# Kernel tuning notes

Measured on AMD Instinct MI355X. Metric: run time of the kernel, lower is better.

Reference implementation:

```python
import jax, jax.numpy as jnp
import numpy as np
from jax import lax

M = 4194304      # total ray samples
N_RAYS = 16384   # number of rays
INTERVAL = 0.5
ALPHA_INIT = 1e-6


def setup_inputs() -> dict:
    key = jax.random.key(0)
    k1, k2, k3 = jax.random.split(key, 3)
    density = jax.random.normal(k1, (M,), dtype=jnp.float32)
    rgb_raw = jax.random.normal(k2, (M, 3), dtype=jnp.float32)
    # act_shift buffer: log(1/(1-alpha_init) - 1)
    shift = jnp.full((1,), np.log(1.0 / (1.0 - ALPHA_INIT) - 1.0), dtype=jnp.float32)
    ray_id = jnp.sort(jax.random.randint(k3, (M,), 0, N_RAYS, dtype=jnp.int32))
    return {"density": density, "rgb_raw": rgb_raw, "shift": shift,
            "ray_id": ray_id, "N": N_RAYS}


def _seg_comb(a, b):
    # associative operator for segmented product scan: (prod, reset_flag)
    pa, fa = a
    pb, fb = b
    return jnp.where(fb, pb, pa * pb), fa | fb


def reference(density, rgb_raw, shift, ray_id, N):
    # Raw2Alpha: alpha = 1 - exp(-softplus(density + shift) * interval)
    s = jax.nn.softplus(density + shift[0]) * INTERVAL   # [M], >= 0
    alpha = -jnp.expm1(-s)                                # 1 - exp(-s), stable
    om = jnp.exp(-s)                                      # 1 - alpha, exact

    # Alphas2Weights: per-ray transmittance scan over variable-length segments.
    first = jnp.concatenate([jnp.ones((1,), bool), ray_id[1:] != ray_id[:-1]])
    # inclusive segmented cumprod of (1 - alpha)
    Tin, _ = lax.associative_scan(_seg_comb, (om, first))
    # exclusive transmittance: T_i = prod of (1-alpha_j) for j earlier in same ray
    T = jnp.where(first, 1.0, jnp.concatenate([jnp.ones((1,), om.dtype), Tin[:-1]]))
    weights = alpha * T                                   # [M]
    # leftover transmittance per ray (1 for rays with no samples)
    alphainv_last = jax.ops.segment_prod(om, ray_id, num_segments=N)  # [N]

    # alpha compositing of colors against a white background
    rgb = jax.nn.sigmoid(rgb_raw)                          # [M,3]
    rgb_marched = (jax.ops.segment_sum(weights[:, None] * rgb, ray_id, num_segments=N)
                   + alphainv_last[:, None])               # [N,3]
    return rgb_marched
```

## Files before the change

kernel.cpp:

```cpp
#include <hip/hip_runtime.h>
#include <math.h>


#define INTERVAL 0.5f

__global__ __launch_bounds__(256) void voxel_march_kernel(
    const float* __restrict__ density,
    const float* __restrict__ rgb_raw,
    const float* __restrict__ shift,
    const int*   __restrict__ ray_id,
    float* __restrict__ out,
    int M, int N)
{
    const int lane = threadIdx.x & 63;
    const int wave = threadIdx.x >> 6;
    const int ray  = blockIdx.x * 4 + wave;
    if (ray >= N) return;

    const float sh = shift[0];

    int target = ray + (lane >= 32 ? 1 : 0);
    int lo = 0, len = M;
    while (len > 0) {
        int half = len >> 1;
        int mid  = lo + half;
        if (ray_id[mid] < target) { lo = mid + 1; len -= half + 1; }
        else                      { len = half; }
    }
    const int begin = __shfl(lo, 0, 64);
    const int end   = __shfl(lo, 32, 64);

    float carry = 1.0f;
    float acc0 = 0.0f, acc1 = 0.0f, acc2 = 0.0f;

    for (int base = (begin & ~3); base < end; base += 256) {
        const int b4 = base + 4 * lane;

        float d0, d1, d2, d3;
        float r[12];

        if (b4 >= begin && b4 + 3 < end) {
            const float4 dd = *(const float4*)(density + b4);
            d0 = dd.x; d1 = dd.y; d2 = dd.z; d3 = dd.w;
            const float4* rp = (const float4*)(rgb_raw + 3 * b4);
            float4 a0 = rp[0], a1 = rp[1], a2 = rp[2];
            r[0]=a0.x; r[1]=a0.y; r[2]=a0.z; r[3]=a0.w;
            r[4]=a1.x; r[5]=a1.y; r[6]=a1.z; r[7]=a1.w;
            r[8]=a2.x; r[9]=a2.y; r[10]=a2.z; r[11]=a2.w;
        } else {
            #pragma unroll
            for (int k = 0; k < 4; ++k) {
                const int j = b4 + k;
                const bool act = (j >= begin) && (j < end);
                float dk = act ? density[j] : -1e30f;
                if (k == 0) d0 = dk; else if (k == 1) d1 = dk;
                else if (k == 2) d2 = dk; else d3 = dk;
                r[3*k+0] = act ? rgb_raw[3*j+0] : 0.0f;
                r[3*k+1] = act ? rgb_raw[3*j+1] : 0.0f;
                r[3*k+2] = act ? rgb_raw[3*j+2] : 0.0f;
            }
        }

        const float om0 = __builtin_amdgcn_rsqf(1.0f + __expf(d0 + sh));
        const float om1 = __builtin_amdgcn_rsqf(1.0f + __expf(d1 + sh));
        const float om2 = __builtin_amdgcn_rsqf(1.0f + __expf(d2 + sh));
        const float om3 = __builtin_amdgcn_rsqf(1.0f + __expf(d3 + sh));
        const float al0 = 1.0f - om0, al1 = 1.0f - om1;
        const float al2 = 1.0f - om2, al3 = 1.0f - om3;

        const float lp = (om0 * om1) * (om2 * om3);
        float p = lp;
        #pragma unroll
        for (int off = 1; off < 64; off <<= 1) {
            float q = __shfl_up(p, off, 64);
            if (lane >= off) p *= q;
        }
        float excl = __shfl_up(p, 1, 64);
        if (lane == 0) excl = 1.0f;

        float t = carry * excl;
        const float w0 = al0 * t; t *= om0;
        const float w1 = al1 * t; t *= om1;
        const float w2 = al2 * t; t *= om2;
        const float w3 = al3 * t;

        acc0 += w0 * __builtin_amdgcn_rcpf(1.0f + __expf(-r[0]))
              + w1 * __builtin_amdgcn_rcpf(1.0f + __expf(-r[3]))
              + w2 * __builtin_amdgcn_rcpf(1.0f + __expf(-r[6]))
              + w3 * __builtin_amdgcn_rcpf(1.0f + __expf(-r[9]));
        acc1 += w0 * __builtin_amdgcn_rcpf(1.0f + __expf(-r[1]))
              + w1 * __builtin_amdgcn_rcpf(1.0f + __expf(-r[4]))
              + w2 * __builtin_amdgcn_rcpf(1.0f + __expf(-r[7]))
              + w3 * __builtin_amdgcn_rcpf(1.0f + __expf(-r[10]));
        acc2 += w0 * __builtin_amdgcn_rcpf(1.0f + __expf(-r[2]))
              + w1 * __builtin_amdgcn_rcpf(1.0f + __expf(-r[5]))
              + w2 * __builtin_amdgcn_rcpf(1.0f + __expf(-r[8]))
              + w3 * __builtin_amdgcn_rcpf(1.0f + __expf(-r[11]));

        carry *= __shfl(p, 63, 64);
    }

    #pragma unroll
    for (int off = 32; off > 0; off >>= 1) {
        acc0 += __shfl_down(acc0, off, 64);
        acc1 += __shfl_down(acc1, off, 64);
        acc2 += __shfl_down(acc2, off, 64);
    }

    if (lane == 0) {
        out[3 * ray + 0] = acc0 + carry;
        out[3 * ray + 1] = acc1 + carry;
        out[3 * ray + 2] = acc2 + carry;
    }
}

extern "C" void kernel_launch(void* const* d_in, const int* in_sizes, int n_in,
                              void* d_out, int out_size, void* d_ws, size_t ws_size,
                              hipStream_t stream)
{
    const float* density = (const float*)d_in[0];
    const float* rgb_raw = (const float*)d_in[1];
    const float* shift   = (const float*)d_in[2];
    const int*   ray_id  = (const int*)d_in[3];
    float* out = (float*)d_out;

    const int M = in_sizes[0];
    const int N = out_size / 3;

    const int rays_per_block = 4;
    const int blocks = (N + rays_per_block - 1) / rays_per_block;
    voxel_march_kernel<<<blocks, 256, 0, stream>>>(density, rgb_raw, shift, ray_id,
                                                   out, M, N);
}
```

Before: 129.8 us.

## Precompute ray segment starts in a separate kernel and use branchless vector loads

Adds a pre-pass kernel that writes each ray's start offset into workspace, replacing the per-wave binary search over ray_id. The main loop now always does clamped float4 loads and masks invalid samples with selects instead of a scalar fallback path. This removes the dependent global-memory latency chain of the search and the divergent edge handling. In exchange it adds a second launch, a full read of ray_id, and a workspace dependency with a fallback when the workspace is too small.

```diff
diff --git a/kernel.cpp b/kernel.cpp
--- a/kernel.cpp
+++ b/kernel.cpp
@@ -2,13 +2,30 @@
 #include <math.h>
 
 
-#define INTERVAL 0.5f
+__device__ __forceinline__ float sigm(float x) {
+    return __builtin_amdgcn_rcpf(1.0f + __expf(-x));
+}
 
+__global__ __launch_bounds__(256) void seg_starts_kernel(
+    const int* __restrict__ ray_id, int* __restrict__ starts, int M, int N)
+{
+    const int i = blockIdx.x * 256 + threadIdx.x;
+    if (i >= M) return;
+    const int cur  = ray_id[i];
+    const int prev = (i == 0) ? -1 : ray_id[i - 1];
+    for (int r = prev + 1; r <= cur; ++r) starts[r] = i;
+    if (i == M - 1) {
+        for (int r = cur + 1; r <= N; ++r) starts[r] = M;
+    }
+}
+
+template <bool USE_STARTS>
 __global__ __launch_bounds__(256) void voxel_march_kernel(
     const float* __restrict__ density,
     const float* __restrict__ rgb_raw,
     const float* __restrict__ shift,
     const int*   __restrict__ ray_id,
+    const int*   __restrict__ starts,
     float* __restrict__ out,
     int M, int N)
 {
@@ -19,47 +36,42 @@
 
     const float sh = shift[0];
 
-    int target = ray + (lane >= 32 ? 1 : 0);
-    int lo = 0, len = M;
-    while (len > 0) {
-        int half = len >> 1;
-        int mid  = lo + half;
-        if (ray_id[mid] < target) { lo = mid + 1; len -= half + 1; }
-        else                      { len = half; }
+    int begin, end;
+    if (USE_STARTS) {
+        begin = starts[ray];
+        end   = starts[ray + 1];
+    } else {
+        int target = ray + (lane >= 32 ? 1 : 0);
+        int lo = 0, len = M;
+        while (len > 0) {
+            int half = len >> 1;
+            int mid  = lo + half;
+            if (ray_id[mid] < target) { lo = mid + 1; len -= half + 1; }
+            else                      { len = half; }
+        }
+        begin = __shfl(lo, 0, 64);
+        end   = __shfl(lo, 32, 64);
     }
-    const int begin = __shfl(lo, 0, 64);
-    const int end   = __shfl(lo, 32, 64);
 
     float carry = 1.0f;
     float acc0 = 0.0f, acc1 = 0.0f, acc2 = 0.0f;
 
     for (int base = (begin & ~3); base < end; base += 256) {
         const int b4 = base + 4 * lane;
+        const int ba = min(b4, M - 4);
 
-        float d0, d1, d2, d3;
-        float r[12];
+        const float4 dd = *(const float4*)(density + ba);
+        const float4* rp = (const float4*)(rgb_raw + 3 * ba);
+        const float4 c0 = rp[0], c1 = rp[1], c2 = rp[2];
 
-        if (b4 >= begin && b4 + 3 < end) {
-            const float4 dd = *(const float4*)(density + b4);
-            d0 = dd.x; d1 = dd.y; d2 = dd.z; d3 = dd.w;
-            const float4* rp = (const float4*)(rgb_raw + 3 * b4);
-            float4 a0 = rp[0], a1 = rp[1], a2 = rp[2];
-            r[0]=a0.x; r[1]=a0.y; r[2]=a0.z; r[3]=a0.w;
-            r[4]=a1.x; r[5]=a1.y; r[6]=a1.z; r[7]=a1.w;
-            r[8]=a2.x; r[9]=a2.y; r[10]=a2.z; r[11]=a2.w;
-        } else {
-            #pragma unroll
-            for (int k = 0; k < 4; ++k) {
-                const int j = b4 + k;
-                const bool act = (j >= begin) && (j < end);
-                float dk = act ? density[j] : -1e30f;
-                if (k == 0) d0 = dk; else if (k == 1) d1 = dk;
-                else if (k == 2) d2 = dk; else d3 = dk;
-                r[3*k+0] = act ? rgb_raw[3*j+0] : 0.0f;
-                r[3*k+1] = act ? rgb_raw[3*j+1] : 0.0f;
-                r[3*k+2] = act ? rgb_raw[3*j+2] : 0.0f;
-            }
-        }
+        const bool v0 = (b4 + 0 >= begin) & (b4 + 0 < end);
+        const bool v1 = (b4 + 1 >= begin) & (b4 + 1 < end);
+        const bool v2 = (b4 + 2 >= begin) & (b4 + 2 < end);
+        const bool v3 = (b4 + 3 >= begin) & (b4 + 3 < end);
+        const float d0 = v0 ? dd.x : -1e30f;
+        const float d1 = v1 ? dd.y : -1e30f;
+        const float d2 = v2 ? dd.z : -1e30f;
+        const float d3 = v3 ? dd.w : -1e30f;
 
         const float om0 = __builtin_amdgcn_rsqf(1.0f + __expf(d0 + sh));
         const float om1 = __builtin_amdgcn_rsqf(1.0f + __expf(d1 + sh));
@@ -84,18 +96,9 @@
         const float w2 = al2 * t; t *= om2;
         const float w3 = al3 * t;
 
-        acc0 += w0 * __builtin_amdgcn_rcpf(1.0f + __expf(-r[0]))
-              + w1 * __builtin_amdgcn_rcpf(1.0f + __expf(-r[3]))
-              + w2 * __builtin_amdgcn_rcpf(1.0f + __expf(-r[6]))
-              + w3 * __builtin_amdgcn_rcpf(1.0f + __expf(-r[9]));
-        acc1 += w0 * __builtin_amdgcn_rcpf(1.0f + __expf(-r[1]))
-              + w1 * __builtin_amdgcn_rcpf(1.0f + __expf(-r[4]))
-              + w2 * __builtin_amdgcn_rcpf(1.0f + __expf(-r[7]))
-              + w3 * __builtin_amdgcn_rcpf(1.0f + __expf(-r[10]));
-        acc2 += w0 * __builtin_amdgcn_rcpf(1.0f + __expf(-r[2]))
-              + w1 * __builtin_amdgcn_rcpf(1.0f + __expf(-r[5]))
-              + w2 * __builtin_amdgcn_rcpf(1.0f + __expf(-r[8]))
-              + w3 * __builtin_amdgcn_rcpf(1.0f + __expf(-r[11]));
+        acc0 += w0 * sigm(c0.x) + w1 * sigm(c0.w) + w2 * sigm(c1.z) + w3 * sigm(c2.y);
+        acc1 += w0 * sigm(c0.y) + w1 * sigm(c1.x) + w2 * sigm(c1.w) + w3 * sigm(c2.z);
+        acc2 += w0 * sigm(c0.z) + w1 * sigm(c1.y) + w2 * sigm(c2.x) + w3 * sigm(c2.w);
 
         carry *= __shfl(p, 63, 64);
     }
@@ -129,6 +132,14 @@
 
     const int rays_per_block = 4;
     const int blocks = (N + rays_per_block - 1) / rays_per_block;
-    voxel_march_kernel<<<blocks, 256, 0, stream>>>(density, rgb_raw, shift, ray_id,
-                                                   out, M, N);
+
+    if (ws_size >= (size_t)(N + 1) * sizeof(int)) {
+        int* starts = (int*)d_ws;
+        seg_starts_kernel<<<(M + 255) / 256, 256, 0, stream>>>(ray_id, starts, M, N);
+        voxel_march_kernel<true><<<blocks, 256, 0, stream>>>(
+            density, rgb_raw, shift, ray_id, starts, out, M, N);
+    } else {
+        voxel_march_kernel<false><<<blocks, 256, 0, stream>>>(
+            density, rgb_raw, shift, ray_id, (const int*)nullptr, out, M, N);
+    }
 }
```

Result: faster. 112.8 us (-13.1%).
